# Optimization experiments

Measured on AMD Instinct MI355X. Metric: run time of the kernel, lower is better.

The kernel has to match this reference:

```python
import jax, jax.numpy as jnp
import numpy as np

NUM_HEADS = 16
EPS = 1e-5


def setup_inputs() -> dict:
    key = jax.random.key(0)
    ks = jax.random.split(key, 9)
    B, S, D = 2, 2048, 1024
    s = 1.0 / np.sqrt(D)
    return {
        "x": jax.random.normal(ks[0], (B, S, D), dtype=jnp.float32),
        "Wq": jax.random.uniform(ks[1], (D, D), jnp.float32, -s, s),
        "bq": jax.random.uniform(ks[2], (D,), jnp.float32, -s, s),
        "Wk": jax.random.uniform(ks[3], (D, D), jnp.float32, -s, s),
        "bk": jax.random.uniform(ks[4], (D,), jnp.float32, -s, s),
        "Wv": jax.random.uniform(ks[5], (D, D), jnp.float32, -s, s),
        "bv": jax.random.uniform(ks[6], (D,), jnp.float32, -s, s),
        "Wo": jax.random.uniform(ks[7], (D, D), jnp.float32, -s, s),
        "bo": jax.random.uniform(ks[8], (D,), jnp.float32, -s, s),
    }


def reference(x, Wq, bq, Wk, bk, Wv, bv, Wo, bo):
    B, S, D = x.shape
    H = NUM_HEADS
    hd = D // H
    # projections -> [B, H, S, hd]
    def proj(W, b):
        return (x @ W + b).reshape(B, S, H, hd).transpose(0, 2, 1, 3)
    Q = proj(Wq, bq)
    K = proj(Wk, bk)
    V = proj(Wv, bv)
    scores = jnp.einsum("bhqd,bhkd->bhqk", Q, K) / jnp.sqrt(jnp.float32(hd))
    attn = jax.nn.softmax(scores, axis=-1)  # dropout is identity in eval mode
    out = jnp.einsum("bhqk,bhkd->bhqd", attn, V)
    out = out.transpose(0, 2, 1, 3).reshape(B, S, D)
    out = jax.nn.relu(out @ Wo + bo)
    mu = jnp.mean(out, axis=-1, keepdims=True)
    var = jnp.var(out, axis=-1, keepdims=True)
    return (out - mu) * jax.lax.rsqrt(var + EPS)
```

## Files before the change

kernel.cpp:

```cpp
#include <hip/hip_runtime.h>
#include <hip/hip_bf16.h>
#include <math.h>

#define Bb 2
#define Ss 2048
#define Dd 1024
#define Hh 16
#define HD 64
#define Mm (Bb*Ss)

typedef __attribute__((ext_vector_type(8))) short bf8_t;
typedef __attribute__((ext_vector_type(4))) float f4_t;
typedef __attribute__((ext_vector_type(2))) unsigned u2_t;

#define LOG2E 1.4426950408889634f

#define AS1 __attribute__((address_space(1)))
#define AS3 __attribute__((address_space(3)))

__device__ __forceinline__ void gl2lds16(const void* g, void* l) {
    __builtin_amdgcn_global_load_lds((const AS1 unsigned int*)g,
                                     (AS3 unsigned int*)l, 16, 0, 0);
}
__device__ __forceinline__ short bfr(float f) {
    __hip_bfloat16 h = __float2bfloat16(f);
    return *reinterpret_cast<short*>(&h);
}
__device__ __forceinline__ unsigned pkbf16(float a, float b) {
    const unsigned ua = __builtin_bit_cast(unsigned, a) + 0x8000u;
    const unsigned ub = __builtin_bit_cast(unsigned, b) + 0x8000u;
    return __builtin_amdgcn_perm(ub, ua, 0x07060302u);
}

__global__ __launch_bounds__(256)
void cast_x(const float* __restrict__ x, __hip_bfloat16* __restrict__ xh)
{
    const size_t i = ((size_t)blockIdx.x * 256 + threadIdx.x) * 8;
    const float4 a = *(const float4*)&x[i];
    const float4 b = *(const float4*)&x[i + 4];
    bf8_t o;
    o[0] = bfr(a.x); o[1] = bfr(a.y); o[2] = bfr(a.z); o[3] = bfr(a.w);
    o[4] = bfr(b.x); o[5] = bfr(b.y); o[6] = bfr(b.z); o[7] = bfr(b.w);
    *(bf8_t*)&xh[i] = o;
}

__global__ __launch_bounds__(256)
void tcast4(const float* __restrict__ w0, const float* __restrict__ w1,
            const float* __restrict__ w2, const float* __restrict__ w3,
            __hip_bfloat16* __restrict__ dst)
{
    const float* W = (blockIdx.z == 0) ? w0 : (blockIdx.z == 1) ? w1
                   : (blockIdx.z == 2) ? w2 : w3;
    __hip_bfloat16* Wt = dst + (size_t)blockIdx.z * Dd * Dd;
    __shared__ float t[32][33];
    const int n0 = blockIdx.x * 32, k0 = blockIdx.y * 32;
    const int tx = threadIdx.x & 31, ty = threadIdx.x >> 5;
    #pragma unroll
    for (int rr = 0; rr < 4; ++rr)
        t[ty + rr*8][tx] = W[(size_t)(k0 + ty + rr*8) * Dd + n0 + tx];
    __syncthreads();
    #pragma unroll
    for (int rr = 0; rr < 4; ++rr)
        Wt[(size_t)(n0 + ty + rr*8) * Dd + k0 + tx] =
            __float2bfloat16(t[tx][ty + rr*8]);
}

template<int MODE>
__global__ __launch_bounds__(256)
void gemm_mfma(const __hip_bfloat16* __restrict__ A,
               const __hip_bfloat16* __restrict__ Bt,
               const float* __restrict__ b0, const float* __restrict__ b1,
               const float* __restrict__ b2,
               __hip_bfloat16* __restrict__ Qh, __hip_bfloat16* __restrict__ Kh,
               __hip_bfloat16* __restrict__ Vt, float* __restrict__ Ro,
               int M, int N, int lda, int kLoop)
{
    __shared__ __hip_bfloat16 As[2][128 * 32];
    __shared__ __hip_bfloat16 Bs[2][128 * 32];

    const int tid  = threadIdx.x;
    const int wave = tid >> 6;
    const int lane = tid & 63;
    const int llo  = lane & 15;
    const int lhi  = lane >> 4;
    const int wm   = wave & 1;
    const int wn   = wave >> 1;
    const int row0 = blockIdx.y * 128;
    const int col0 = blockIdx.x * 128;
    const int z    = blockIdx.z;

    size_t aoff[2], boff[2];
    int    loff[2];
    #pragma unroll
    for (int p = 0; p < 2; ++p) {
        const int g = p * 256 + wave * 64 + lane;
        const int r = g >> 2, kc = (g & 3) * 8;
        aoff[p] = (size_t)(row0 + r) * lda + kc;
        boff[p] = (size_t)(col0 + r) * lda + kc;
        loff[p] = (p * 256 + wave * 64) * 16;
    }
    const __hip_bfloat16* Acur = A  + (size_t)z * kLoop;
    const __hip_bfloat16* Bcur = Bt + (size_t)z * kLoop;

    auto stage = [&](int buf) {
        #pragma unroll
        for (int p = 0; p < 2; ++p) {
            gl2lds16(Acur + aoff[p], (char*)&As[buf][0] + loff[p]);
            gl2lds16(Bcur + boff[p], (char*)&Bs[buf][0] + loff[p]);
        }
        Acur += 32; Bcur += 32;
    };

    f4_t acc[4][4] = {};
    const int nIt = kLoop >> 5;

    stage(0);
    for (int kt = 0; kt < nIt; ++kt) {
        const int buf = kt & 1;
        __syncthreads();
        if (kt + 1 < nIt) stage(buf ^ 1);

        bf8_t a[4], b[4];
        #pragma unroll
        for (int i = 0; i < 4; ++i)
            a[i] = *(const bf8_t*)&As[buf][(wm*64 + i*16 + llo) * 32 + lhi*8];
        #pragma unroll
        for (int j = 0; j < 4; ++j)
            b[j] = *(const bf8_t*)&Bs[buf][(wn*64 + j*16 + llo) * 32 + lhi*8];
        #pragma unroll
        for (int i = 0; i < 4; ++i)
            #pragma unroll
            for (int j = 0; j < 4; ++j)
                acc[i][j] = __builtin_amdgcn_mfma_f32_16x16x32_bf16(
                    a[i], b[j], acc[i][j], 0, 0, 0);
    }

    if (MODE == 0) {
        const int sel   = col0 >> 10;
        const int cbase = col0 & 1023;
        const float scale = (sel == 0) ? 0.125f * LOG2E : 1.0f;
        const float* bp = (sel == 0) ? b0 : (sel == 1) ? b1 : b2;
        __hip_bfloat16* outQK = (sel == 0) ? Qh : Kh;
        #pragma unroll
        for (int i = 0; i < 4; ++i) {
            #pragma unroll
            for (int r = 0; r < 4; ++r) {
                const int m  = row0 + wm*64 + i*16 + lhi*4 + r;
                const int b_ = m >> 11, s_ = m & (Ss - 1);
                #pragma unroll
                for (int j = 0; j < 4; ++j) {
                    const int col = cbase + wn*64 + j*16 + llo;
                    const int h_  = col >> 6, e_ = col & 63;
                    const float v = (acc[i][j][r] + bp[col]) * scale;
                    const __hip_bfloat16 hv = __float2bfloat16(v);
                    if (sel < 2)
                        outQK[((size_t)(b_*Hh + h_)*Ss + s_)*HD + e_] = hv;
                    else
                        Vt[((size_t)(b_*Hh + h_)*HD + e_)*Ss + s_] = hv;
                }
            }
        }
    } else {
        float* Roz = Ro + (size_t)z * M * N;
        #pragma unroll
        for (int i = 0; i < 4; ++i) {
            #pragma unroll
            for (int r = 0; r < 4; ++r) {
                const int m = row0 + wm*64 + i*16 + lhi*4 + r;
                #pragma unroll
                for (int j = 0; j < 4; ++j) {
                    const int col = col0 + wn*64 + j*16 + llo;
                    Roz[(size_t)m * N + col] = acc[i][j][r];
                }
            }
        }
    }
}

__global__ __launch_bounds__(128, 2)
void attn_mfma(const __hip_bfloat16* __restrict__ Qh,
               const __hip_bfloat16* __restrict__ Kh,
               const __hip_bfloat16* __restrict__ Vt,
               __hip_bfloat16* __restrict__ Ah)
{
    const int b    = blockIdx.z;
    const int h    = blockIdx.y;
    const int wave = threadIdx.x >> 6;
    const int lane = threadIdx.x & 63;
    const int llo  = lane & 15;
    const int lhi  = lane >> 4;
    const int qb   = blockIdx.x * 64 + wave * 32;

    const size_t base = ((size_t)(b*Hh + h)) * Ss * HD;

    __shared__ __hip_bfloat16 Ks[2][2 * 64 * 32];
    __shared__ __hip_bfloat16 Vs[2][2 * 64 * 32];
    __shared__ __hip_bfloat16 Pl[2][32 * 64];
    __hip_bfloat16* Pw = &Pl[wave][0];

    int koff[4], voff[4], loff[4];
    #pragma unroll
    for (int it = 0; it < 4; ++it) {
        const int g  = it*128 + wave*64 + lane;
        const int hf = g >> 8;
        const int rr = (g >> 2) & 63;
        const int c8 = (g & 3) * 8;
        koff[it] = rr*HD + hf*32 + c8;
        voff[it] = rr*Ss + hf*32 + c8;
        loff[it] = (it*128 + wave*64) * 16;
    }
    const __hip_bfloat16* Kcur = Kh + base;
    const __hip_bfloat16* Vcur = Vt + base;

    auto stage = [&](int buf) {
        #pragma unroll
        for (int it = 0; it < 4; ++it) {
            gl2lds16(Kcur + koff[it], (char*)&Ks[buf][0] + loff[it]);
            gl2lds16(Vcur + voff[it], (char*)&Vs[buf][0] + loff[it]);
        }
        Kcur += 64 * HD;
        Vcur += 64;
    };

    bf8_t qf[2][2];
    #pragma unroll
    for (int s = 0; s < 2; ++s)
        #pragma unroll
        for (int d = 0; d < 2; ++d)
            qf[s][d] = *(const bf8_t*)&Qh[base + (size_t)(qb + 16*s + llo)*HD + 32*d + lhi*8];

    f4_t o_[2][4];
    float lacc[2];
    #pragma unroll
    for (int s = 0; s < 2; ++s) {
        #pragma unroll
        for (int n = 0; n < 4; ++n) o_[s][n] = (f4_t){0.f,0.f,0.f,0.f};
        lacc[s] = 0.f;
    }

    const f4_t zf = {0.f,0.f,0.f,0.f};
    const int llo7 = llo & 7;

    stage(0);

    for (int t = 0; t < Ss/64; ++t) {
        const int buf = t & 1;
        __syncthreads();
        if (t + 1 < Ss/64) stage(buf ^ 1);

        bf8_t kf[4][2];
        #pragma unroll
        for (int kc = 0; kc < 4; ++kc)
            #pragma unroll
            for (int d = 0; d < 2; ++d)
                kf[kc][d] = *(const bf8_t*)&Ks[buf][d*2048 + (kc*16 + llo)*32 + lhi*8];

        f4_t sacc[2][4];
        #pragma unroll
        for (int s = 0; s < 2; ++s)
            #pragma unroll
            for (int kc = 0; kc < 4; ++kc) {
                sacc[s][kc] = __builtin_amdgcn_mfma_f32_16x16x32_bf16(kf[kc][0], qf[s][0], zf, 0, 0, 0);
                sacc[s][kc] = __builtin_amdgcn_mfma_f32_16x16x32_bf16(kf[kc][1], qf[s][1], sacc[s][kc], 0, 0, 0);
            }

        #pragma unroll
        for (int s = 0; s < 2; ++s) {
            #pragma unroll
            for (int kc = 0; kc < 4; ++kc) {
                const float p0 = exp2f(sacc[s][kc][0]);
                const float p1 = exp2f(sacc[s][kc][1]);
                const float p2 = exp2f(sacc[s][kc][2]);
                const float p3 = exp2f(sacc[s][kc][3]);
                lacc[s] += (p0 + p1) + (p2 + p3);
                const u2_t pk = { pkbf16(p0, p1), pkbf16(p2, p3) };
                const int phys = (2*kc + (lhi >> 1)) ^ llo7;
                *(u2_t*)&Pw[(16*s + llo)*64 + phys*8 + (lhi & 1)*4] = pk;
            }
        }
        asm volatile("s_waitcnt lgkmcnt(0)" ::: "memory");

        #pragma unroll
        for (int d = 0; d < 2; ++d) {
            bf8_t pf[2];
            #pragma unroll
            for (int s = 0; s < 2; ++s)
                pf[s] = *(const bf8_t*)&Pw[(16*s + llo)*64 + (((4*d + lhi) ^ llo7) << 3)];
            #pragma unroll
            for (int nc = 0; nc < 4; ++nc) {
                const bf8_t vf = *(const bf8_t*)&Vs[buf][d*2048 + (nc*16 + llo)*32 + lhi*8];
                #pragma unroll
                for (int s = 0; s < 2; ++s)
                    o_[s][nc] = __builtin_amdgcn_mfma_f32_16x16x32_bf16(pf[s], vf, o_[s][nc], 0, 0, 0);
            }
        }
    }

    #pragma unroll
    for (int s = 0; s < 2; ++s) {
        lacc[s] += __shfl_xor(lacc[s], 16);
        lacc[s] += __shfl_xor(lacc[s], 32);
    }

    #pragma unroll
    for (int s = 0; s < 2; ++s) {
        #pragma unroll
        for (int r = 0; r < 4; ++r) {
            const float lv  = __shfl(lacc[s], 4*lhi + r);
            const float inv = 1.0f / lv;
            const int q = qb + 16*s + 4*lhi + r;
            __hip_bfloat16* orow = &Ah[((size_t)(b*Ss) + q)*Dd + h*HD + llo];
            #pragma unroll
            for (int nc = 0; nc < 4; ++nc)
                orow[16*nc] = __float2bfloat16(o_[s][nc][r] * inv);
        }
    }
}

__global__ __launch_bounds__(256)
void layernorm(const float* __restrict__ P0, const float* __restrict__ P1,
               const float* __restrict__ bias, float* __restrict__ out)
{
    const int row = blockIdx.x;
    const int c = threadIdx.x;
    const float4 a  = ((const float4*)(P0 + (size_t)row*Dd))[c];
    const float4 b  = ((const float4*)(P1 + (size_t)row*Dd))[c];
    const float4 bb = ((const float4*)bias)[c];
    float4 v;
    v.x = fmaxf(a.x + b.x + bb.x, 0.0f);
    v.y = fmaxf(a.y + b.y + bb.y, 0.0f);
    v.z = fmaxf(a.z + b.z + bb.z, 0.0f);
    v.w = fmaxf(a.w + b.w + bb.w, 0.0f);

    float s  = v.x + v.y + v.z + v.w;
    float ss = v.x*v.x + v.y*v.y + v.z*v.z + v.w*v.w;
    #pragma unroll
    for (int off = 32; off > 0; off >>= 1) {
        s  += __shfl_down(s,  off);
        ss += __shfl_down(ss, off);
    }
    __shared__ float rs[4], rss[4];
    const int wid = c >> 6, lid = c & 63;
    if (lid == 0) { rs[wid] = s; rss[wid] = ss; }
    __syncthreads();
    s  = rs[0] + rs[1] + rs[2] + rs[3];
    ss = rss[0] + rss[1] + rss[2] + rss[3];
    const float mean = s * (1.0f / Dd);
    const float var  = ss * (1.0f / Dd) - mean * mean;
    const float rstd = rsqrtf(var + 1e-5f);
    float4 o;
    o.x = (v.x - mean) * rstd;
    o.y = (v.y - mean) * rstd;
    o.z = (v.z - mean) * rstd;
    o.w = (v.w - mean) * rstd;
    ((float4*)(out + (size_t)row*Dd))[c] = o;
}

extern "C" void kernel_launch(void* const* d_in, const int* in_sizes, int n_in,
                              void* d_out, int out_size, void* d_ws, size_t ws_size,
                              hipStream_t stream)
{
    const float* x  = (const float*)d_in[0];
    const float* Wq = (const float*)d_in[1];
    const float* bq = (const float*)d_in[2];
    const float* Wk = (const float*)d_in[3];
    const float* bk = (const float*)d_in[4];
    const float* Wv = (const float*)d_in[5];
    const float* bv = (const float*)d_in[6];
    const float* Wo = (const float*)d_in[7];
    const float* bo = (const float*)d_in[8];
    float* out = (float*)d_out;

    __hip_bfloat16* Xh    = (__hip_bfloat16*)d_ws;
    __hip_bfloat16* Wqkvt = Xh    + (size_t)Mm*Dd;
    __hip_bfloat16* Wot   = Wqkvt + (size_t)3*Dd*Dd;
    __hip_bfloat16* Ah    = Wot   + (size_t)Dd*Dd;
    __hip_bfloat16* Qh    = Ah    + (size_t)Mm*Dd;
    __hip_bfloat16* Kh    = Qh    + (size_t)Mm*Dd;
    __hip_bfloat16* Vt    = Kh    + (size_t)Mm*Dd;
    float*          Rb    = (float*)Qh;

    const dim3 blk(256);
    cast_x<<<dim3((Mm*Dd)/(256*8)), blk, 0, stream>>>(x, Xh);
    tcast4<<<dim3(32, 32, 4), blk, 0, stream>>>(Wq, Wk, Wv, Wo, Wqkvt);

    gemm_mfma<0><<<dim3(3*Dd/128, Mm/128), blk, 0, stream>>>(
        Xh, Wqkvt, bq, bk, bv, Qh, Kh, Vt, nullptr, Mm, 3*Dd, Dd, Dd);
    attn_mfma<<<dim3(Ss/64, Hh, Bb), dim3(128), 0, stream>>>(Qh, Kh, Vt, Ah);
    gemm_mfma<1><<<dim3(Dd/128, Mm/128, 2), blk, 0, stream>>>(
        Ah, Wot, nullptr, nullptr, nullptr, nullptr, nullptr, nullptr, Rb,
        Mm, Dd, Dd, Dd/2);
    layernorm<<<dim3(Mm), blk, 0, stream>>>(Rb, Rb + (size_t)Mm*Dd, bo, out);
}
```

Baseline: 231.3 us.

## Merge prep casts, stage V transpose via LDS, replace split-K out GEMM

Merges the x cast and the weight transpose-cast into one prep launch. The V-projection epilogue now goes through an LDS tile so it can write the transposed V with 16-byte stores instead of scattered 2-byte ones. The split-K output GEMM is replaced by a 64x64-tile full-K GEMM that applies the bias and ReLU in its epilogue, which drops the second partial buffer and its read in layernorm. It also swaps exp2f for the hardware exp2 intrinsic in attention. The trade-off is smaller output-GEMM tiles with less operand reuse, plus extra LDS and a barrier in the V epilogue.

```diff
diff --git a/kernel.cpp b/kernel.cpp
--- a/kernel.cpp
+++ b/kernel.cpp
@@ -31,52 +31,54 @@
     const unsigned ub = __builtin_bit_cast(unsigned, b) + 0x8000u;
     return __builtin_amdgcn_perm(ub, ua, 0x07060302u);
 }
+__device__ __forceinline__ float fexp2(float x) {
+    return __builtin_amdgcn_exp2f(x);
+}
 
 __global__ __launch_bounds__(256)
-void cast_x(const float* __restrict__ x, __hip_bfloat16* __restrict__ xh)
-{
-    const size_t i = ((size_t)blockIdx.x * 256 + threadIdx.x) * 8;
-    const float4 a = *(const float4*)&x[i];
-    const float4 b = *(const float4*)&x[i + 4];
-    bf8_t o;
-    o[0] = bfr(a.x); o[1] = bfr(a.y); o[2] = bfr(a.z); o[3] = bfr(a.w);
-    o[4] = bfr(b.x); o[5] = bfr(b.y); o[6] = bfr(b.z); o[7] = bfr(b.w);
-    *(bf8_t*)&xh[i] = o;
+void prep(const float* __restrict__ x,
+          const float* __restrict__ w0, const float* __restrict__ w1,
+          const float* __restrict__ w2, const float* __restrict__ w3,
+          __hip_bfloat16* __restrict__ Wt4, __hip_bfloat16* __restrict__ Xh)
+{
+    const int z = blockIdx.z;
+    if (z < 4) {
+        const float* W = (z == 0) ? w0 : (z == 1) ? w1 : (z == 2) ? w2 : w3;
+        __hip_bfloat16* Wt = Wt4 + (size_t)z * Dd * Dd;
+        __shared__ float t[32][33];
+        const int n0 = blockIdx.x * 32, k0 = blockIdx.y * 32;
+        const int tx = threadIdx.x & 31, ty = threadIdx.x >> 5;
+        #pragma unroll
+        for (int rr = 0; rr < 4; ++rr)
+            t[ty + rr*8][tx] = W[(size_t)(k0 + ty + rr*8) * Dd + n0 + tx];
+        __syncthreads();
+        #pragma unroll
+        for (int rr = 0; rr < 4; ++rr)
+            Wt[(size_t)(n0 + ty + rr*8) * Dd + k0 + tx] =
+                __float2bfloat16(t[tx][ty + rr*8]);
+    } else {
+        const int bid = (z - 4) * 1024 + blockIdx.y * 32 + blockIdx.x;
+        const size_t i = ((size_t)bid * 256 + threadIdx.x) * 8;
+        const float4 a = *(const float4*)&x[i];
+        const float4 b = *(const float4*)&x[i + 4];
+        bf8_t o;
+        o[0] = bfr(a.x); o[1] = bfr(a.y); o[2] = bfr(a.z); o[3] = bfr(a.w);
+        o[4] = bfr(b.x); o[5] = bfr(b.y); o[6] = bfr(b.z); o[7] = bfr(b.w);
+        *(bf8_t*)&Xh[i] = o;
+    }
 }
 
 __global__ __launch_bounds__(256)
-void tcast4(const float* __restrict__ w0, const float* __restrict__ w1,
-            const float* __restrict__ w2, const float* __restrict__ w3,
-            __hip_bfloat16* __restrict__ dst)
-{
-    const float* W = (blockIdx.z == 0) ? w0 : (blockIdx.z == 1) ? w1
-                   : (blockIdx.z == 2) ? w2 : w3;
-    __hip_bfloat16* Wt = dst + (size_t)blockIdx.z * Dd * Dd;
-    __shared__ float t[32][33];
-    const int n0 = blockIdx.x * 32, k0 = blockIdx.y * 32;
-    const int tx = threadIdx.x & 31, ty = threadIdx.x >> 5;
-    #pragma unroll
-    for (int rr = 0; rr < 4; ++rr)
-        t[ty + rr*8][tx] = W[(size_t)(k0 + ty + rr*8) * Dd + n0 + tx];
-    __syncthreads();
-    #pragma unroll
-    for (int rr = 0; rr < 4; ++rr)
-        Wt[(size_t)(n0 + ty + rr*8) * Dd + k0 + tx] =
-            __float2bfloat16(t[tx][ty + rr*8]);
-}
-
-template<int MODE>
-__global__ __launch_bounds__(256)
-void gemm_mfma(const __hip_bfloat16* __restrict__ A,
-               const __hip_bfloat16* __restrict__ Bt,
-               const float* __restrict__ b0, const float* __restrict__ b1,
-               const float* __restrict__ b2,
-               __hip_bfloat16* __restrict__ Qh, __hip_bfloat16* __restrict__ Kh,
-               __hip_bfloat16* __restrict__ Vt, float* __restrict__ Ro,
-               int M, int N, int lda, int kLoop)
-{
-    __shared__ __hip_bfloat16 As[2][128 * 32];
-    __shared__ __hip_bfloat16 Bs[2][128 * 32];
+void gemm_qkv(const __hip_bfloat16* __restrict__ A,
+              const __hip_bfloat16* __restrict__ Bt,
+              const float* __restrict__ b0, const float* __restrict__ b1,
+              const float* __restrict__ b2,
+              __hip_bfloat16* __restrict__ Qh, __hip_bfloat16* __restrict__ Kh,
+              __hip_bfloat16* __restrict__ Vt)
+{
+    __shared__ __align__(16) char pool[34816];
+    __hip_bfloat16* As = (__hip_bfloat16*)pool;
+    __hip_bfloat16* Bs = As + 2 * 128 * 32;
 
     const int tid  = threadIdx.x;
     const int wave = tid >> 6;
@@ -87,7 +89,6 @@
     const int wn   = wave >> 1;
     const int row0 = blockIdx.y * 128;
     const int col0 = blockIdx.x * 128;
-    const int z    = blockIdx.z;
 
     size_t aoff[2], boff[2];
     int    loff[2];
@@ -95,38 +96,36 @@
     for (int p = 0; p < 2; ++p) {
         const int g = p * 256 + wave * 64 + lane;
         const int r = g >> 2, kc = (g & 3) * 8;
-        aoff[p] = (size_t)(row0 + r) * lda + kc;
-        boff[p] = (size_t)(col0 + r) * lda + kc;
+        aoff[p] = (size_t)(row0 + r) * Dd + kc;
+        boff[p] = (size_t)(col0 + r) * Dd + kc;
         loff[p] = (p * 256 + wave * 64) * 16;
     }
-    const __hip_bfloat16* Acur = A  + (size_t)z * kLoop;
-    const __hip_bfloat16* Bcur = Bt + (size_t)z * kLoop;
+    const __hip_bfloat16* Acur = A;
+    const __hip_bfloat16* Bcur = Bt;
 
     auto stage = [&](int buf) {
         #pragma unroll
         for (int p = 0; p < 2; ++p) {
-            gl2lds16(Acur + aoff[p], (char*)&As[buf][0] + loff[p]);
-            gl2lds16(Bcur + boff[p], (char*)&Bs[buf][0] + loff[p]);
+            gl2lds16(Acur + aoff[p], (char*)As + buf*8192 + loff[p]);
+            gl2lds16(Bcur + boff[p], (char*)Bs + buf*8192 + loff[p]);
         }
         Acur += 32; Bcur += 32;
     };
 
     f4_t acc[4][4] = {};
-    const int nIt = kLoop >> 5;
-
     stage(0);
-    for (int kt = 0; kt < nIt; ++kt) {
+    for (int kt = 0; kt < 32; ++kt) {
         const int buf = kt & 1;
         __syncthreads();
-        if (kt + 1 < nIt) stage(buf ^ 1);
+        if (kt + 1 < 32) stage(buf ^ 1);
 
         bf8_t a[4], b[4];
         #pragma unroll
         for (int i = 0; i < 4; ++i)
-            a[i] = *(const bf8_t*)&As[buf][(wm*64 + i*16 + llo) * 32 + lhi*8];
+            a[i] = *(const bf8_t*)&As[buf*4096 + (wm*64 + i*16 + llo) * 32 + lhi*8];
         #pragma unroll
         for (int j = 0; j < 4; ++j)
-            b[j] = *(const bf8_t*)&Bs[buf][(wn*64 + j*16 + llo) * 32 + lhi*8];
+            b[j] = *(const bf8_t*)&Bs[buf*4096 + (wn*64 + j*16 + llo) * 32 + lhi*8];
         #pragma unroll
         for (int i = 0; i < 4; ++i)
             #pragma unroll
@@ -135,11 +134,11 @@
                     a[i], b[j], acc[i][j], 0, 0, 0);
     }
 
-    if (MODE == 0) {
-        const int sel   = col0 >> 10;
-        const int cbase = col0 & 1023;
+    const int sel   = col0 >> 10;
+    const int cbase = col0 & 1023;
+    if (sel < 2) {
         const float scale = (sel == 0) ? 0.125f * LOG2E : 1.0f;
-        const float* bp = (sel == 0) ? b0 : (sel == 1) ? b1 : b2;
+        const float* bp = (sel == 0) ? b0 : b1;
         __hip_bfloat16* outQK = (sel == 0) ? Qh : Kh;
         #pragma unroll
         for (int i = 0; i < 4; ++i) {
@@ -152,27 +151,36 @@
                     const int col = cbase + wn*64 + j*16 + llo;
                     const int h_  = col >> 6, e_ = col & 63;
                     const float v = (acc[i][j][r] + bp[col]) * scale;
-                    const __hip_bfloat16 hv = __float2bfloat16(v);
-                    if (sel < 2)
-                        outQK[((size_t)(b_*Hh + h_)*Ss + s_)*HD + e_] = hv;
-                    else
-                        Vt[((size_t)(b_*Hh + h_)*HD + e_)*Ss + s_] = hv;
+                    outQK[((size_t)(b_*Hh + h_)*Ss + s_)*HD + e_] = __float2bfloat16(v);
                 }
             }
         }
     } else {
-        float* Roz = Ro + (size_t)z * M * N;
-        #pragma unroll
-        for (int i = 0; i < 4; ++i) {
+        __syncthreads();
+        __hip_bfloat16* Ls = (__hip_bfloat16*)pool;
+        float bv[4];
+        #pragma unroll
+        for (int j = 0; j < 4; ++j) bv[j] = b2[cbase + wn*64 + j*16 + llo];
+        #pragma unroll
+        for (int i = 0; i < 4; ++i)
             #pragma unroll
             for (int r = 0; r < 4; ++r) {
-                const int m = row0 + wm*64 + i*16 + lhi*4 + r;
+                const int ml = wm*64 + i*16 + lhi*4 + r;
                 #pragma unroll
-                for (int j = 0; j < 4; ++j) {
-                    const int col = col0 + wn*64 + j*16 + llo;
-                    Roz[(size_t)m * N + col] = acc[i][j][r];
-                }
-            }
+                for (int j = 0; j < 4; ++j)
+                    Ls[(wn*64 + j*16 + llo)*136 + ml] =
+                        __float2bfloat16(acc[i][j][r] + bv[j]);
+            }
+        __syncthreads();
+        const int b_ = row0 >> 11;
+        const int sb = row0 & (Ss - 1);
+        #pragma unroll
+        for (int p = 0; p < 8; ++p) {
+            const int cl = p*16 + (tid >> 4);
+            const int m  = (tid & 15) * 8;
+            const bf8_t v = *(const bf8_t*)&Ls[cl*136 + m];
+            const int cc = cbase + cl;
+            *(bf8_t*)&Vt[((size_t)(b_*Hh + (cc >> 6))*HD + (cc & 63))*Ss + sb + m] = v;
         }
     }
 }
@@ -268,10 +276,10 @@
         for (int s = 0; s < 2; ++s) {
             #pragma unroll
             for (int kc = 0; kc < 4; ++kc) {
-                const float p0 = exp2f(sacc[s][kc][0]);
-                const float p1 = exp2f(sacc[s][kc][1]);
-                const float p2 = exp2f(sacc[s][kc][2]);
-                const float p3 = exp2f(sacc[s][kc][3]);
+                const float p0 = fexp2(sacc[s][kc][0]);
+                const float p1 = fexp2(sacc[s][kc][1]);
+                const float p2 = fexp2(sacc[s][kc][2]);
+                const float p3 = fexp2(sacc[s][kc][3]);
                 lacc[s] += (p0 + p1) + (p2 + p3);
                 const u2_t pk = { pkbf16(p0, p1), pkbf16(p2, p3) };
                 const int phys = (2*kc + (lhi >> 1)) ^ llo7;
@@ -318,20 +326,77 @@
 }
 
 __global__ __launch_bounds__(256)
-void layernorm(const float* __restrict__ P0, const float* __restrict__ P1,
-               const float* __restrict__ bias, float* __restrict__ out)
+void gemm_out(const __hip_bfloat16* __restrict__ A,
+              const __hip_bfloat16* __restrict__ Bt,
+              const float* __restrict__ bias, float* __restrict__ Ro)
+{
+    __shared__ __hip_bfloat16 As[2][64 * 32];
+    __shared__ __hip_bfloat16 Bs[2][64 * 32];
+
+    const int tid  = threadIdx.x;
+    const int wave = tid >> 6;
+    const int lane = tid & 63;
+    const int llo  = lane & 15;
+    const int lhi  = lane >> 4;
+    const int wm   = wave & 1;
+    const int wn   = wave >> 1;
+    const int row0 = blockIdx.y * 64;
+    const int col0 = blockIdx.x * 64;
+
+    const int gr = tid >> 2, gkc = (tid & 3) * 8;
+    const size_t aoff = (size_t)(row0 + gr) * Dd + gkc;
+    const size_t boff = (size_t)(col0 + gr) * Dd + gkc;
+    const int loff = (wave * 64) * 16;
+    const __hip_bfloat16* Acur = A;
+    const __hip_bfloat16* Bcur = Bt;
+
+    auto stage = [&](int buf) {
+        gl2lds16(Acur + aoff, (char*)&As[buf][0] + loff);
+        gl2lds16(Bcur + boff, (char*)&Bs[buf][0] + loff);
+        Acur += 32; Bcur += 32;
+    };
+
+    f4_t acc[2][2] = {};
+    stage(0);
+    for (int kt = 0; kt < 32; ++kt) {
+        const int buf = kt & 1;
+        __syncthreads();
+        if (kt + 1 < 32) stage(buf ^ 1);
+
+        bf8_t a[2], b[2];
+        #pragma unroll
+        for (int i = 0; i < 2; ++i)
+            a[i] = *(const bf8_t*)&As[buf][(wm*32 + i*16 + llo) * 32 + lhi*8];
+        #pragma unroll
+        for (int j = 0; j < 2; ++j)
+            b[j] = *(const bf8_t*)&Bs[buf][(wn*32 + j*16 + llo) * 32 + lhi*8];
+        #pragma unroll
+        for (int i = 0; i < 2; ++i)
+            #pragma unroll
+            for (int j = 0; j < 2; ++j)
+                acc[i][j] = __builtin_amdgcn_mfma_f32_16x16x32_bf16(
+                    a[i], b[j], acc[i][j], 0, 0, 0);
+    }
+
+    #pragma unroll
+    for (int i = 0; i < 2; ++i) {
+        #pragma unroll
+        for (int r = 0; r < 4; ++r) {
+            const int m = row0 + wm*32 + i*16 + lhi*4 + r;
+            #pragma unroll
+            for (int j = 0; j < 2; ++j) {
+                const int col = col0 + wn*32 + j*16 + llo;
+                Ro[(size_t)m * Dd + col] = fmaxf(acc[i][j][r] + bias[col], 0.0f);
+            }
+        }
+    }
+}
+
+__global__ __launch_bounds__(256)
+void layernorm(const float* __restrict__ X, float* __restrict__ out)
 {
     const int row = blockIdx.x;
-    const int c = threadIdx.x;
-    const float4 a  = ((const float4*)(P0 + (size_t)row*Dd))[c];
-    const float4 b  = ((const float4*)(P1 + (size_t)row*Dd))[c];
-    const float4 bb = ((const float4*)bias)[c];
-    float4 v;
-    v.x = fmaxf(a.x + b.x + bb.x, 0.0f);
-    v.y = fmaxf(a.y + b.y + bb.y, 0.0f);
-    v.z = fmaxf(a.z + b.z + bb.z, 0.0f);
-    v.w = fmaxf(a.w + b.w + bb.w, 0.0f);
-
+    const float4 v = ((const float4*)(X + (size_t)row*Dd))[threadIdx.x];
     float s  = v.x + v.y + v.z + v.w;
     float ss = v.x*v.x + v.y*v.y + v.z*v.z + v.w*v.w;
     #pragma unroll
@@ -340,7 +405,7 @@
         ss += __shfl_down(ss, off);
     }
     __shared__ float rs[4], rss[4];
-    const int wid = c >> 6, lid = c & 63;
+    const int wid = threadIdx.x >> 6, lid = threadIdx.x & 63;
     if (lid == 0) { rs[wid] = s; rss[wid] = ss; }
     __syncthreads();
     s  = rs[0] + rs[1] + rs[2] + rs[3];
@@ -353,7 +418,7 @@
     o.y = (v.y - mean) * rstd;
     o.z = (v.z - mean) * rstd;
     o.w = (v.w - mean) * rstd;
-    ((float4*)(out + (size_t)row*Dd))[c] = o;
+    ((float4*)(out + (size_t)row*Dd))[threadIdx.x] = o;
 }
 
 extern "C" void kernel_launch(void* const* d_in, const int* in_sizes, int n_in,
@@ -380,15 +445,10 @@
     __hip_bfloat16* Vt    = Kh    + (size_t)Mm*Dd;
     float*          Rb    = (float*)Qh;
 
-    const dim3 blk(256);
-    cast_x<<<dim3((Mm*Dd)/(256*8)), blk, 0, stream>>>(x, Xh);
-    tcast4<<<dim3(32, 32, 4), blk, 0, stream>>>(Wq, Wk, Wv, Wo, Wqkvt);
-
-    gemm_mfma<0><<<dim3(3*Dd/128, Mm/128), blk, 0, stream>>>(
-        Xh, Wqkvt, bq, bk, bv, Qh, Kh, Vt, nullptr, Mm, 3*Dd, Dd, Dd);
+    prep<<<dim3(32, 32, 6), dim3(256), 0, stream>>>(x, Wq, Wk, Wv, Wo, Wqkvt, Xh);
+    gemm_qkv<<<dim3(3*Dd/128, Mm/128), dim3(256), 0, stream>>>(
+        Xh, Wqkvt, bq, bk, bv, Qh, Kh, Vt);
     attn_mfma<<<dim3(Ss/64, Hh, Bb), dim3(128), 0, stream>>>(Qh, Kh, Vt, Ah);
-    gemm_mfma<1><<<dim3(Dd/128, Mm/128, 2), blk, 0, stream>>>(
-        Ah, Wot, nullptr, nullptr, nullptr, nullptr, nullptr, nullptr, Rb,
-        Mm, Dd, Dd, Dd/2);
-    layernorm<<<dim3(Mm), blk, 0, stream>>>(Rb, Rb + (size_t)Mm*Dd, bo, out);
-}
+    gemm_out<<<dim3(Dd/64, Mm/64), dim3(256), 0, stream>>>(Ah, Wot, bo, Rb);
+    layernorm<<<dim3(Mm), dim3(256), 0, stream>>>(Rb, out);
+}
```

Measured after the change: 221.5 us. 4.2% less time.
